# Optimization experiments

Measured on AMD Instinct MI355X. Metric: run time of the kernel, lower is better.

Reference implementation:

```python
import jax, jax.numpy as jnp
import numpy as np

N, M, K, C, FF, H, OUT = 20000, 80000, 48, 64, 256, 4, 64


def _lin(x, w, b):
    return x @ w.T + b


def _bn(x, g, b, eps=1e-5):
    mu = x.mean(0)
    var = x.var(0)
    return (x - mu) * jax.lax.rsqrt(var + eps) * g + b


def setup_inputs() -> dict:
    key = jax.random.key(0)
    ks = jax.random.split(key, 24)
    voxel_features = jax.random.normal(ks[0], (M, C), jnp.float32)
    voxel_coords = jax.random.normal(ks[1], (M, 3), jnp.float32)
    query_coords = jax.random.normal(ks[2], (N, 3), jnp.float32)
    idx = jax.random.randint(ks[3], (N, K), 0, M)
    drop = jax.random.uniform(ks[4], (N, K)) < 0.1
    drop = drop.at[:, 0].set(False)  # keep >=1 valid key per query
    key_indices = jnp.where(drop, -1, idx)
    s = 0.05
    p = lambda i, shp: jax.random.normal(ks[i], shp, jnp.float32) * s
    return {
        "voxel_features": voxel_features,
        "voxel_coords": voxel_coords,
        "query_coords": query_coords,
        "key_indices": key_indices,
        "q_w": p(5, (C, 3)), "q_b": p(6, (C,)),
        "kpos_w": p(7, (C, 3)), "kpos_b": p(8, (C,)),
        "in_w": p(9, (3 * C, C)), "in_b": p(10, (3 * C,)),
        "out_w": p(11, (C, C)), "out_b": p(12, (C,)),
        "lin1_w": p(13, (FF, C)), "lin1_b": p(14, (FF,)),
        "lin2_w": p(15, (C, FF)), "lin2_b": p(16, (C,)),
        "norm_g": jnp.ones((C,), jnp.float32), "norm_b": jnp.zeros((C,), jnp.float32),
        "outl_w": p(17, (OUT, C)), "outl_b": p(18, (OUT,)),
        "obn_g": jnp.ones((OUT,), jnp.float32), "obn_b": jnp.zeros((OUT,), jnp.float32),
    }


def reference(voxel_features, voxel_coords, query_coords, key_indices,
              q_w, q_b, kpos_w, kpos_b, in_w, in_b, out_w, out_b,
              lin1_w, lin1_b, lin2_w, lin2_b, norm_g, norm_b,
              outl_w, outl_b, obn_g, obn_b):
    hd = C // H
    mask = key_indices < 0                      # (N,K) padded keys
    safe = jnp.where(mask, 0, key_indices)
    key_feats = voxel_features[safe]            # (N,K,C) hash-gather
    key_coords = voxel_coords[safe]             # (N,K,3)
    # query positional projection
    q_feat = jax.nn.relu(_lin(query_coords, q_w, q_b))          # (N,C)
    # relative coords + key positional conv1d(kernel=1) == linear on coord dim
    rel = key_coords - query_coords[:, None, :]                  # (N,K,3)
    key_feats = key_feats + jax.nn.relu(_lin(rel, kpos_w, kpos_b))
    # multihead attention, query length 1 per voxel
    Wq, Wk, Wv = jnp.split(in_w, 3, axis=0)
    bq, bk, bv = jnp.split(in_b, 3)
    q = (_lin(q_feat, Wq, bq) / jnp.sqrt(jnp.float32(hd))).reshape(N, H, hd)
    k = _lin(key_feats, Wk, bk).reshape(N, K, H, hd)
    v = _lin(key_feats, Wv, bv).reshape(N, K, H, hd)
    scores = jnp.einsum('nhd,nkhd->nhk', q, k)
    scores = jnp.where(mask[:, None, :], -jnp.inf, scores)
    attn = jax.nn.softmax(scores, axis=-1)
    ctx = jnp.einsum('nhk,nkhd->nhd', attn, v).reshape(N, C)
    att = _lin(ctx, out_w, out_b)                                # (N,C)
    # FFN + residual
    x = att + _lin(jax.nn.relu(_lin(att, lin1_w, lin1_b)), lin2_w, lin2_b)
    x = _bn(x, norm_g, norm_b)
    # output layer: Linear -> BN -> ReLU
    x = jax.nn.relu(_bn(_lin(x, outl_w, outl_b), obn_g, obn_b))
    return x
```

## Files before the change

kernel.cpp:

```cpp
#include <hip/hip_runtime.h>
#include <math.h>

#define N_Q 20000
#define KK 48
#define CC 64
#define FFD 256

#define TW_WOT   0
#define TW_WVT   4096
#define U_L1     16384
#define U_L2     32768
#define U_OL     49152
#define U_WQ     53248
#define U_WK     57344
#define ST_OFF   32768
#define M_OFF    33024
#define VF_OFF   2593024

typedef short bf16x8 __attribute__((ext_vector_type(8)));
typedef float f32x4  __attribute__((ext_vector_type(4)));

__device__ __forceinline__ unsigned f2bf(float f) {
    unsigned u = __float_as_uint(f);
    return (u + 0x7fffu + ((u >> 16) & 1u)) >> 16;
}
__device__ __forceinline__ unsigned pk2(float a, float b) {
    return f2bf(a) | (f2bf(b) << 16);
}
__device__ __forceinline__ float bflo(unsigned u) { return __uint_as_float(u << 16); }
__device__ __forceinline__ float bfhi(unsigned u) { return __uint_as_float(u & 0xffff0000u); }
__device__ __forceinline__ bf16x8 ldfrag(const unsigned short* p) {
    return *(const bf16x8*)p;
}

__global__ void prep_all(const float* __restrict__ in_w,
                         const float* __restrict__ out_w,
                         const float* __restrict__ lin1_w,
                         const float* __restrict__ lin2_w,
                         const float* __restrict__ outl_w,
                         const float* __restrict__ vfeat,
                         float* __restrict__ tw,
                         unsigned short* __restrict__ wsu,
                         unsigned short* __restrict__ vfeat_bf,
                         float* __restrict__ stats)
{
    int t = blockIdx.x * 256 + threadIdx.x;
    if (t < 1280000) {
        float4 v = ((const float4*)vfeat)[t];
        uint2 p; p.x = pk2(v.x, v.y); p.y = pk2(v.z, v.w);
        ((uint2*)vfeat_bf)[t] = p;
        return;
    }
    int u = t - 1280000;
    if (u < 4096) {
        int c = u >> 6, j = u & 63;
        tw[TW_WOT + j*64 + c] = out_w[c*64 + j];
    } else if (u < 8192) {
        int i = u - 4096, cp = i >> 6, c = i & 63;
        tw[TW_WVT + cp*64 + c] = in_w[(128 + c)*64 + cp];
    } else if (u < 24576) {
        int i = u - 8192;
        wsu[U_L1 + i] = (unsigned short)f2bf(lin1_w[i]);
    } else if (u < 40960) {
        int i = u - 24576;
        wsu[U_L2 + i] = (unsigned short)f2bf(lin2_w[i]);
    } else if (u < 45056) {
        int i = u - 40960;
        wsu[U_OL + i] = (unsigned short)f2bf(outl_w[i]);
    } else if (u < 49152) {
        int i = u - 45056;
        wsu[U_WQ + i] = (unsigned short)f2bf(in_w[i]);
    } else if (u < 57344) {
        int v = u - 49152;
        int h = v >> 11, rem = v & 2047, j = rem >> 5, k = rem & 31;
        unsigned short val = 0;
        if (k < 16) val = (unsigned short)f2bf(in_w[(64 + h*16 + k)*64 + j]);
        wsu[U_WK + v] = val;
    } else if (u < 57600) {
        stats[u - 57344] = 0.0f;
    }
}

__global__ __launch_bounds__(256) void m_kernel(
    const float* __restrict__ qcoord, const float* __restrict__ q_w,
    const float* __restrict__ q_b, const float* __restrict__ in_b,
    const unsigned short* __restrict__ wsu, unsigned short* __restrict__ M_all)
{
    __shared__ __align__(16) unsigned short sQF[80*72];
    __shared__ __align__(16) unsigned short sQ[80*72];
    int t = threadIdx.x, base = blockIdx.x * 80;
    int colq = (t*4) & 63;
    float qwv[12];
    #pragma unroll
    for (int j = 0; j < 12; ++j) qwv[j] = q_w[colq*3 + j];
    float4 qb4 = *(const float4*)&q_b[colq];
    #pragma unroll
    for (int i = 0; i < 5; ++i) {
        int e = i*1024 + t*4, r = e >> 6, n = base + r;
        float c0 = qcoord[n*3], c1 = qcoord[n*3+1], c2 = qcoord[n*3+2];
        float f0 = fmaxf(fmaf(qwv[2],  c2, fmaf(qwv[1],  c1, fmaf(qwv[0], c0, qb4.x))), 0.f);
        float f1 = fmaxf(fmaf(qwv[5],  c2, fmaf(qwv[4],  c1, fmaf(qwv[3], c0, qb4.y))), 0.f);
        float f2 = fmaxf(fmaf(qwv[8],  c2, fmaf(qwv[7],  c1, fmaf(qwv[6], c0, qb4.z))), 0.f);
        float f3 = fmaxf(fmaf(qwv[11], c2, fmaf(qwv[10], c1, fmaf(qwv[9], c0, qb4.w))), 0.f);
        uint2 p; p.x = pk2(f0, f1); p.y = pk2(f2, f3);
        *(uint2*)&sQF[r*72 + colq] = p;
    }
    int w = t >> 6, lane = t & 63, l16 = lane & 15, quad = lane >> 4;
    bf16x8 qbf[2], kbf[4];
    #pragma unroll
    for (int ks = 0; ks < 2; ++ks)
        qbf[ks] = ldfrag(&wsu[U_WQ + (w*16 + l16)*64 + ks*32 + quad*8]);
    #pragma unroll
    for (int nb = 0; nb < 4; ++nb)
        kbf[nb] = ldfrag(&wsu[U_WK + w*2048 + (nb*16 + l16)*32 + quad*8]);
    __syncthreads();

    int cq = w*16 + l16;
    float bq = in_b[cq];
    #pragma unroll
    for (int mb = 0; mb < 5; ++mb) {
        bf16x8 a0 = ldfrag(&sQF[(mb*16 + l16)*72 + quad*8]);
        bf16x8 a1 = ldfrag(&sQF[(mb*16 + l16)*72 + 32 + quad*8]);
        f32x4 acc = {0.f, 0.f, 0.f, 0.f};
        acc = __builtin_amdgcn_mfma_f32_16x16x32_bf16(a0, qbf[0], acc, 0, 0, 0);
        acc = __builtin_amdgcn_mfma_f32_16x16x32_bf16(a1, qbf[1], acc, 0, 0, 0);
        #pragma unroll
        for (int reg = 0; reg < 4; ++reg) {
            int row = mb*16 + quad*4 + reg;
            sQ[row*72 + cq] = (unsigned short)f2bf((acc[reg] + bq) * 0.25f);
        }
    }
    #pragma unroll
    for (int mb = 0; mb < 5; ++mb) {
        bf16x8 a = {0,0,0,0,0,0,0,0};
        if (quad < 2) a = ldfrag(&sQ[(mb*16 + l16)*72 + w*16 + quad*8]);
        f32x4 acc[4];
        #pragma unroll
        for (int nb = 0; nb < 4; ++nb) {
            f32x4 z = {0.f, 0.f, 0.f, 0.f};
            acc[nb] = __builtin_amdgcn_mfma_f32_16x16x32_bf16(a, kbf[nb], z, 0, 0, 0);
        }
        #pragma unroll
        for (int nb = 0; nb < 4; ++nb)
            #pragma unroll
            for (int reg = 0; reg < 4; ++reg) {
                int r = base + mb*16 + quad*4 + reg, j = nb*16 + l16;
                M_all[(size_t)r*256 + w*64 + j] = (unsigned short)f2bf(acc[nb][reg]);
            }
    }
}

__global__ __launch_bounds__(64, 4) void attn_kernel(
    const unsigned short* __restrict__ vfeat_bf, const float* __restrict__ vcoord,
    const float* __restrict__ qcoord, const int* __restrict__ kidx,
    const float* __restrict__ kpos_w, const float* __restrict__ kpos_b,
    const float* __restrict__ in_b, const float* __restrict__ out_b,
    const float* __restrict__ tw, const unsigned short* __restrict__ M_all,
    float* __restrict__ att_out)
{
    __shared__ __align__(16) unsigned short skf[KK*72];
    __shared__ __align__(16) float reg1[256];
    int n = blockIdx.x, c = threadIdx.x;
    int l16 = c & 15, h = c >> 4;
    float* sM   = reg1;
    float* sP   = reg1;
    float* sctx = reg1 + 192;
    float* sT   = (float*)skf;

    {
        uint2 mu = ((const uint2*)(M_all + (size_t)n*256))[c];
        float4 mf;
        mf.x = bflo(mu.x); mf.y = bfhi(mu.x);
        mf.z = bflo(mu.y); mf.w = bfhi(mu.y);
        *(float4*)&sM[h*64 + 4*l16] = mf;
    }

    float qc0 = qcoord[n*3+0], qc1 = qcoord[n*3+1], qc2 = qcoord[n*3+2];

    int kread = c < 48 ? c : 47;
    int idxv = kidx[(size_t)n*KK + kread];
    int sfe = idxv < 0 ? 0 : idxv;
    float rl0 = vcoord[sfe*3+0] - qc0;
    float rl1 = vcoord[sfe*3+1] - qc1;
    float rl2 = vcoord[sfe*3+2] - qc2;

    float4 wA  = *(const float4*)(kpos_w + 12*l16 + 0);
    float4 wB  = *(const float4*)(kpos_w + 12*l16 + 4);
    float4 wC  = *(const float4*)(kpos_w + 12*l16 + 8);
    float4 kb4 = *(const float4*)(kpos_b + 4*l16);

    uint2 fv[12];
    #pragma unroll
    for (int i = 0; i < 12; ++i) {
        int row = 4*i + h;
        int si = __shfl(idxv, row);
        si = si < 0 ? 0 : si;
        fv[i] = *(const uint2*)(vfeat_bf + (size_t)si*64 + 4*l16);
    }
    #pragma unroll
    for (int i = 0; i < 12; ++i) {
        int row = 4*i + h;
        float rr0 = __shfl(rl0, row), rr1 = __shfl(rl1, row), rr2 = __shfl(rl2, row);
        float g0 = bflo(fv[i].x), g1 = bfhi(fv[i].x);
        float g2 = bflo(fv[i].y), g3 = bfhi(fv[i].y);
        g0 += fmaxf(fmaf(wA.x, rr0, fmaf(wA.y, rr1, fmaf(wA.z, rr2, kb4.x))), 0.0f);
        g1 += fmaxf(fmaf(wA.w, rr0, fmaf(wB.x, rr1, fmaf(wB.y, rr2, kb4.y))), 0.0f);
        g2 += fmaxf(fmaf(wB.z, rr0, fmaf(wB.w, rr1, fmaf(wC.x, rr2, kb4.z))), 0.0f);
        g3 += fmaxf(fmaf(wC.y, rr0, fmaf(wC.z, rr1, fmaf(wC.w, rr2, kb4.w))), 0.0f);
        uint2 p; p.x = pk2(g0, g1); p.y = pk2(g2, g3);
        *(uint2*)&skf[row*72 + 4*l16] = p;
    }

    int i0 = __shfl(idxv, l16), i1 = __shfl(idxv, l16 + 16), i2 = __shfl(idxv, l16 + 32);
    float S0 = 0, S1 = 0, S2 = 0;
    #pragma unroll
    for (int j8 = 0; j8 < 8; ++j8) {
        uint2 A = *(const uint2*)&skf[ l16       *72 + 8*j8];
        uint2 A2= *(const uint2*)&skf[ l16       *72 + 8*j8 + 4];
        uint2 B = *(const uint2*)&skf[(l16 + 16) *72 + 8*j8];
        uint2 B2= *(const uint2*)&skf[(l16 + 16) *72 + 8*j8 + 4];
        uint2 D = *(const uint2*)&skf[(l16 + 32) *72 + 8*j8];
        uint2 D2= *(const uint2*)&skf[(l16 + 32) *72 + 8*j8 + 4];
        float4 mA = *(const float4*)&sM[h*64 + 8*j8];
        float4 mB = *(const float4*)&sM[h*64 + 8*j8 + 4];
        #pragma unroll
        for (int jj = 0; jj < 8; ++jj) {
            unsigned ua = (jj < 4) ? ((jj < 2) ? A.x : A.y) : ((jj < 6) ? A2.x : A2.y);
            unsigned ub = (jj < 4) ? ((jj < 2) ? B.x : B.y) : ((jj < 6) ? B2.x : B2.y);
            unsigned ud = (jj < 4) ? ((jj < 2) ? D.x : D.y) : ((jj < 6) ? D2.x : D2.y);
            float av = (jj & 1) ? bfhi(ua) : bflo(ua);
            float bv = (jj & 1) ? bfhi(ub) : bflo(ub);
            float dv = (jj & 1) ? bfhi(ud) : bflo(ud);
            float m  = (jj < 4) ? ((jj < 2) ? ((jj & 1) ? mA.y : mA.x) : ((jj & 1) ? mA.w : mA.z))
                                : ((jj < 6) ? ((jj & 1) ? mB.y : mB.x) : ((jj & 1) ? mB.w : mB.z));
            S0 = fmaf(av, m, S0);
            S1 = fmaf(bv, m, S1);
            S2 = fmaf(dv, m, S2);
        }
    }
    if (i0 < 0) S0 = -INFINITY;
    if (i1 < 0) S1 = -INFINITY;
    if (i2 < 0) S2 = -INFINITY;

    float mx = fmaxf(S0, fmaxf(S1, S2));
    #pragma unroll
    for (int off = 8; off >= 1; off >>= 1) mx = fmaxf(mx, __shfl_xor(mx, off, 16));
    float e0 = __expf(S0 - mx), e1 = __expf(S1 - mx), e2 = __expf(S2 - mx);
    float es = e0 + e1 + e2;
    #pragma unroll
    for (int off = 8; off >= 1; off >>= 1) es += __shfl_xor(es, off, 16);
    float rinv = 1.0f / es;
    sP[ l16       *4 + h] = e0 * rinv;
    sP[(l16 + 16) *4 + h] = e1 * rinv;
    sP[(l16 + 32) *4 + h] = e2 * rinv;

    float T0 = 0, T1 = 0, T2 = 0, T3 = 0;
    #pragma unroll 8
    for (int k = 0; k < KK; ++k) {
        float kf = __uint_as_float(((unsigned)skf[k*72 + c]) << 16);
        float4 p = *(const float4*)&sP[k*4];
        T0 = fmaf(p.x, kf, T0); T1 = fmaf(p.y, kf, T1);
        T2 = fmaf(p.z, kf, T2); T3 = fmaf(p.w, kf, T3);
    }
    sT[0*65 + c] = T0; sT[1*65 + c] = T1; sT[2*65 + c] = T2; sT[3*65 + c] = T3;

    const float* WvT = tw + TW_WVT;
    float ctx = in_b[128 + c];
    #pragma unroll 8
    for (int cp = 0; cp < 64; ++cp)
        ctx = fmaf(sT[h*65 + cp], WvT[cp*64 + c], ctx);
    sctx[c] = ctx;

    const float* WoT = tw + TW_WOT;
    float att = out_b[c];
    #pragma unroll 8
    for (int j = 0; j < 64; ++j)
        att = fmaf(sctx[j], WoT[j*64 + c], att);
    att_out[(size_t)n*64 + c] = att;
}

__global__ __launch_bounds__(256) void ffn_kernel(
    const unsigned short* __restrict__ wsu, const float* __restrict__ lin1_b,
    const float* __restrict__ lin2_b, float* __restrict__ att_y,
    float* __restrict__ sum1, float* __restrict__ sumsq1)
{
    __shared__ __align__(16) unsigned short sA[48*72];
    __shared__ __align__(16) unsigned short sH[48*264];
    int t = threadIdx.x, base = blockIdx.x * 48;
    #pragma unroll
    for (int i = 0; i < 3; ++i) {
        int e = i*1024 + t*4, r = e >> 6, col = e & 63;
        int n = base + r;
        uint2 p = {0u, 0u};
        if (n < N_Q) {
            float4 v = *(const float4*)&att_y[(size_t)n*64 + col];
            p.x = pk2(v.x, v.y); p.y = pk2(v.z, v.w);
        }
        *(uint2*)&sA[r*72 + col] = p;
    }
    int w = t >> 6, lane = t & 63, l16 = lane & 15, quad = lane >> 4;
    bf16x8 b1f[2][4], b2f[8];
    #pragma unroll
    for (int ks = 0; ks < 2; ++ks)
        #pragma unroll
        for (int nb = 0; nb < 4; ++nb)
            b1f[ks][nb] = ldfrag(&wsu[U_L1 + (w*64 + nb*16 + l16)*64 + ks*32 + quad*8]);
    #pragma unroll
    for (int ks = 0; ks < 8; ++ks)
        b2f[ks] = ldfrag(&wsu[U_L2 + (w*16 + l16)*256 + ks*32 + quad*8]);
    __syncthreads();

    #pragma unroll
    for (int mb = 0; mb < 3; ++mb) {
        bf16x8 a0 = ldfrag(&sA[(mb*16 + l16)*72 + quad*8]);
        bf16x8 a1 = ldfrag(&sA[(mb*16 + l16)*72 + 32 + quad*8]);
        #pragma unroll
        for (int nb = 0; nb < 4; ++nb) {
            f32x4 acc = {0.f, 0.f, 0.f, 0.f};
            acc = __builtin_amdgcn_mfma_f32_16x16x32_bf16(a0, b1f[0][nb], acc, 0, 0, 0);
            acc = __builtin_amdgcn_mfma_f32_16x16x32_bf16(a1, b1f[1][nb], acc, 0, 0, 0);
            int f = w*64 + nb*16 + l16;
            float bias = lin1_b[f];
            #pragma unroll
            for (int reg = 0; reg < 4; ++reg) {
                int row = mb*16 + quad*4 + reg;
                sH[row*264 + f] = (unsigned short)f2bf(fmaxf(acc[reg] + bias, 0.0f));
            }
        }
    }
    __syncthreads();

    int c = w*16 + l16;
    float lb2 = lin2_b[c];
    float s = 0.f, ss = 0.f;
    #pragma unroll
    for (int mb = 0; mb < 3; ++mb) {
        f32x4 acc = {0.f, 0.f, 0.f, 0.f};
        #pragma unroll
        for (int ks = 0; ks < 8; ++ks) {
            bf16x8 a = ldfrag(&sH[(mb*16 + l16)*264 + ks*32 + quad*8]);
            acc = __builtin_amdgcn_mfma_f32_16x16x32_bf16(a, b2f[ks], acc, 0, 0, 0);
        }
        #pragma unroll
        for (int reg = 0; reg < 4; ++reg) {
            int r = base + mb*16 + quad*4 + reg;
            if (r < N_Q) {
                float y = att_y[(size_t)r*64 + c] + lb2 + acc[reg];
                att_y[(size_t)r*64 + c] = y;
                s += y; ss = fmaf(y, y, ss);
            }
        }
    }
    s  += __shfl_xor(s, 16);  s  += __shfl_xor(s, 32);
    ss += __shfl_xor(ss, 16); ss += __shfl_xor(ss, 32);
    if (lane < 16) {
        atomicAdd(&sum1[c], s);
        atomicAdd(&sumsq1[c], ss);
    }
}

__global__ __launch_bounds__(256) void linout_kernel(
    const unsigned short* __restrict__ wsu, const float* __restrict__ outl_b,
    const float* __restrict__ norm_g, const float* __restrict__ norm_b,
    const float* __restrict__ sum1, const float* __restrict__ sumsq1,
    const float* __restrict__ y, float* __restrict__ z_out,
    float* __restrict__ sum2, float* __restrict__ sumsq2)
{
    __shared__ __align__(16) unsigned short sX[48*72];
    int t = threadIdx.x, base = blockIdx.x * 48;
    int colq = (t*4) & 63;
    const float invN = 1.0f / 20000.0f;
    float4 sm = *(const float4*)&sum1[colq];
    float4 sq = *(const float4*)&sumsq1[colq];
    float4 g  = *(const float4*)&norm_g[colq];
    float4 bb = *(const float4*)&norm_b[colq];
    float mu0 = sm.x*invN, mu1 = sm.y*invN, mu2 = sm.z*invN, mu3 = sm.w*invN;
    float a0 = g.x / sqrtf(fmaf(-mu0, mu0, sq.x*invN) + 1e-5f);
    float a1 = g.y / sqrtf(fmaf(-mu1, mu1, sq.y*invN) + 1e-5f);
    float a2 = g.z / sqrtf(fmaf(-mu2, mu2, sq.z*invN) + 1e-5f);
    float a3 = g.w / sqrtf(fmaf(-mu3, mu3, sq.w*invN) + 1e-5f);
    float b0 = fmaf(-mu0, a0, bb.x), b1 = fmaf(-mu1, a1, bb.y);
    float b2 = fmaf(-mu2, a2, bb.z), b3 = fmaf(-mu3, a3, bb.w);
    #pragma unroll
    for (int i = 0; i < 3; ++i) {
        int e = i*1024 + t*4, r = e >> 6;
        int n = base + r;
        uint2 p = {0u, 0u};
        if (n < N_Q) {
            float4 v = *(const float4*)&y[(size_t)n*64 + colq];
            p.x = pk2(fmaf(v.x, a0, b0), fmaf(v.y, a1, b1));
            p.y = pk2(fmaf(v.z, a2, b2), fmaf(v.w, a3, b3));
        }
        *(uint2*)&sX[r*72 + colq] = p;
    }
    int w = t >> 6, lane = t & 63, l16 = lane & 15, quad = lane >> 4;
    bf16x8 obf[2];
    #pragma unroll
    for (int ks = 0; ks < 2; ++ks)
        obf[ks] = ldfrag(&wsu[U_OL + (w*16 + l16)*64 + ks*32 + quad*8]);
    __syncthreads();

    int co = w*16 + l16;
    float ob = outl_b[co];
    float s = 0.f, ss = 0.f;
    #pragma unroll
    for (int mb = 0; mb < 3; ++mb) {
        bf16x8 x0 = ldfrag(&sX[(mb*16 + l16)*72 + quad*8]);
        bf16x8 x1 = ldfrag(&sX[(mb*16 + l16)*72 + 32 + quad*8]);
        f32x4 acc = {0.f, 0.f, 0.f, 0.f};
        acc = __builtin_amdgcn_mfma_f32_16x16x32_bf16(x0, obf[0], acc, 0, 0, 0);
        acc = __builtin_amdgcn_mfma_f32_16x16x32_bf16(x1, obf[1], acc, 0, 0, 0);
        #pragma unroll
        for (int reg = 0; reg < 4; ++reg) {
            int r = base + mb*16 + quad*4 + reg;
            if (r < N_Q) {
                float zv = acc[reg] + ob;
                z_out[(size_t)r*64 + co] = zv;
                s += zv; ss = fmaf(zv, zv, ss);
            }
        }
    }
    s  += __shfl_xor(s, 16);  s  += __shfl_xor(s, 32);
    ss += __shfl_xor(ss, 16); ss += __shfl_xor(ss, 32);
    if (lane < 16) {
        atomicAdd(&sum2[co], s);
        atomicAdd(&sumsq2[co], ss);
    }
}

__global__ void final_kernel(float* __restrict__ z,
    const float* __restrict__ sum2, const float* __restrict__ sumsq2,
    const float* __restrict__ obn_g, const float* __restrict__ obn_b)
{
    int i = blockIdx.x*blockDim.x + threadIdx.x;
    if (i >= N_Q*64/4) return;
    int o4 = (i*4) & 63;
    float4 sm = *(const float4*)&sum2[o4];
    float4 sq = *(const float4*)&sumsq2[o4];
    float4 g  = *(const float4*)&obn_g[o4];
    float4 b  = *(const float4*)&obn_b[o4];
    const float invN = 1.0f / 20000.0f;
    float mux = sm.x*invN, muy = sm.y*invN, muz = sm.z*invN, muw = sm.w*invN;
    float ax = g.x / sqrtf(fmaf(-mux, mux, sq.x*invN) + 1e-5f);
    float ay = g.y / sqrtf(fmaf(-muy, muy, sq.y*invN) + 1e-5f);
    float az = g.z / sqrtf(fmaf(-muz, muz, sq.z*invN) + 1e-5f);
    float aw = g.w / sqrtf(fmaf(-muw, muw, sq.w*invN) + 1e-5f);
    float4 v = ((float4*)z)[i];
    v.x = fmaxf(fmaf(v.x - mux, ax, b.x), 0.0f);
    v.y = fmaxf(fmaf(v.y - muy, ay, b.y), 0.0f);
    v.z = fmaxf(fmaf(v.z - muz, az, b.z), 0.0f);
    v.w = fmaxf(fmaf(v.w - muw, aw, b.w), 0.0f);
    ((float4*)z)[i] = v;
}

extern "C" void kernel_launch(void* const* d_in, const int* in_sizes, int n_in,
                              void* d_out, int out_size, void* d_ws, size_t ws_size,
                              hipStream_t stream)
{
    const float* vfeat  = (const float*)d_in[0];
    const float* vcoord = (const float*)d_in[1];
    const float* qcoord = (const float*)d_in[2];
    const int*   kidx   = (const int*)d_in[3];
    const float* q_w    = (const float*)d_in[4];
    const float* q_b    = (const float*)d_in[5];
    const float* kpos_w = (const float*)d_in[6];
    const float* kpos_b = (const float*)d_in[7];
    const float* in_w   = (const float*)d_in[8];
    const float* in_b   = (const float*)d_in[9];
    const float* out_w  = (const float*)d_in[10];
    const float* out_b  = (const float*)d_in[11];
    const float* lin1_w = (const float*)d_in[12];
    const float* lin1_b = (const float*)d_in[13];
    const float* lin2_w = (const float*)d_in[14];
    const float* lin2_b = (const float*)d_in[15];
    const float* norm_g = (const float*)d_in[16];
    const float* norm_b = (const float*)d_in[17];
    const float* outl_w = (const float*)d_in[18];
    const float* outl_b = (const float*)d_in[19];
    const float* obn_g  = (const float*)d_in[20];
    const float* obn_b  = (const float*)d_in[21];

    float* ws = (float*)d_ws;
    float* tw = ws;
    unsigned short* wsu = (unsigned short*)ws;
    float* stats = ws + ST_OFF;
    float* sum1 = stats, *sumsq1 = stats + 64, *sum2 = stats + 128, *sumsq2 = stats + 192;
    unsigned short* M_all = (unsigned short*)(ws + M_OFF);
    unsigned short* vfeat_bf = (unsigned short*)(ws + VF_OFF);
    float* xd = (float*)d_out;

    prep_all<<<5225, 256, 0, stream>>>(in_w, out_w, lin1_w, lin2_w, outl_w,
                                       vfeat, tw, wsu, vfeat_bf, stats);
    m_kernel<<<250, 256, 0, stream>>>(qcoord, q_w, q_b, in_b, wsu, M_all);
    attn_kernel<<<N_Q, 64, 0, stream>>>(vfeat_bf, vcoord, qcoord, kidx, kpos_w, kpos_b,
                                        in_b, out_b, tw, M_all, xd);
    ffn_kernel<<<417, 256, 0, stream>>>(wsu, lin1_b, lin2_b, xd, sum1, sumsq1);
    linout_kernel<<<417, 256, 0, stream>>>(wsu, outl_b, norm_g, norm_b, sum1, sumsq1,
                                           xd, xd, sum2, sumsq2);
    final_kernel<<<1250, 256, 0, stream>>>(xd, sum2, sumsq2, obn_g, obn_b);
}
```

Before: 208.6 us.

## Shrink row tiles to raise block count and interleave M layout by head

The m_kernel, ffn_kernel and linout_kernel now process 32 or 16 rows per block instead of 80 or 48, which launches more blocks so the small kernels cover more compute units; the bounds checks go away because 20000 divides evenly. The M matrix is stored with heads interleaved (j*4+h), so attn_kernel writes it contiguously and reads one scalar per step from shared memory instead of selecting from float4 vectors. Weight fragments are reloaded more often in total, and there are more atomics on the statistics buffers. The scalar shared-memory reads may cost more LDS instructions or bank conflicts.

```diff
diff --git a/kernel.cpp b/kernel.cpp
--- a/kernel.cpp
+++ b/kernel.cpp
@@ -86,16 +86,16 @@
     const float* __restrict__ q_b, const float* __restrict__ in_b,
     const unsigned short* __restrict__ wsu, unsigned short* __restrict__ M_all)
 {
-    __shared__ __align__(16) unsigned short sQF[80*72];
-    __shared__ __align__(16) unsigned short sQ[80*72];
-    int t = threadIdx.x, base = blockIdx.x * 80;
+    __shared__ __align__(16) unsigned short sQF[32*72];
+    __shared__ __align__(16) unsigned short sQ[32*72];
+    int t = threadIdx.x, base = blockIdx.x * 32;
     int colq = (t*4) & 63;
     float qwv[12];
     #pragma unroll
     for (int j = 0; j < 12; ++j) qwv[j] = q_w[colq*3 + j];
     float4 qb4 = *(const float4*)&q_b[colq];
     #pragma unroll
-    for (int i = 0; i < 5; ++i) {
+    for (int i = 0; i < 2; ++i) {
         int e = i*1024 + t*4, r = e >> 6, n = base + r;
         float c0 = qcoord[n*3], c1 = qcoord[n*3+1], c2 = qcoord[n*3+2];
         float f0 = fmaxf(fmaf(qwv[2],  c2, fmaf(qwv[1],  c1, fmaf(qwv[0], c0, qb4.x))), 0.f);
@@ -118,7 +118,7 @@
     int cq = w*16 + l16;
     float bq = in_b[cq];
     #pragma unroll
-    for (int mb = 0; mb < 5; ++mb) {
+    for (int mb = 0; mb < 2; ++mb) {
         bf16x8 a0 = ldfrag(&sQF[(mb*16 + l16)*72 + quad*8]);
         bf16x8 a1 = ldfrag(&sQF[(mb*16 + l16)*72 + 32 + quad*8]);
         f32x4 acc = {0.f, 0.f, 0.f, 0.f};
@@ -131,7 +131,7 @@
         }
     }
     #pragma unroll
-    for (int mb = 0; mb < 5; ++mb) {
+    for (int mb = 0; mb < 2; ++mb) {
         bf16x8 a = {0,0,0,0,0,0,0,0};
         if (quad < 2) a = ldfrag(&sQ[(mb*16 + l16)*72 + w*16 + quad*8]);
         f32x4 acc[4];
@@ -145,7 +145,7 @@
             #pragma unroll
             for (int reg = 0; reg < 4; ++reg) {
                 int r = base + mb*16 + quad*4 + reg, j = nb*16 + l16;
-                M_all[(size_t)r*256 + w*64 + j] = (unsigned short)f2bf(acc[nb][reg]);
+                M_all[(size_t)r*256 + j*4 + w] = (unsigned short)f2bf(acc[nb][reg]);
             }
     }
 }
@@ -172,7 +172,7 @@
         float4 mf;
         mf.x = bflo(mu.x); mf.y = bfhi(mu.x);
         mf.z = bflo(mu.y); mf.w = bfhi(mu.y);
-        *(float4*)&sM[h*64 + 4*l16] = mf;
+        *(float4*)&sM[4*c] = mf;
     }
 
     float qc0 = qcoord[n*3+0], qc1 = qcoord[n*3+1], qc2 = qcoord[n*3+2];
@@ -221,8 +221,6 @@
         uint2 B2= *(const uint2*)&skf[(l16 + 16) *72 + 8*j8 + 4];
         uint2 D = *(const uint2*)&skf[(l16 + 32) *72 + 8*j8];
         uint2 D2= *(const uint2*)&skf[(l16 + 32) *72 + 8*j8 + 4];
-        float4 mA = *(const float4*)&sM[h*64 + 8*j8];
-        float4 mB = *(const float4*)&sM[h*64 + 8*j8 + 4];
         #pragma unroll
         for (int jj = 0; jj < 8; ++jj) {
             unsigned ua = (jj < 4) ? ((jj < 2) ? A.x : A.y) : ((jj < 6) ? A2.x : A2.y);
@@ -231,8 +229,7 @@
             float av = (jj & 1) ? bfhi(ua) : bflo(ua);
             float bv = (jj & 1) ? bfhi(ub) : bflo(ub);
             float dv = (jj & 1) ? bfhi(ud) : bflo(ud);
-            float m  = (jj < 4) ? ((jj < 2) ? ((jj & 1) ? mA.y : mA.x) : ((jj & 1) ? mA.w : mA.z))
-                                : ((jj < 6) ? ((jj & 1) ? mB.y : mB.x) : ((jj & 1) ? mB.w : mB.z));
+            float m  = sM[(8*j8 + jj)*4 + h];
             S0 = fmaf(av, m, S0);
             S1 = fmaf(bv, m, S1);
             S2 = fmaf(dv, m, S2);
@@ -284,18 +281,13 @@
     const float* __restrict__ lin2_b, float* __restrict__ att_y,
     float* __restrict__ sum1, float* __restrict__ sumsq1)
 {
-    __shared__ __align__(16) unsigned short sA[48*72];
-    __shared__ __align__(16) unsigned short sH[48*264];
-    int t = threadIdx.x, base = blockIdx.x * 48;
-    #pragma unroll
-    for (int i = 0; i < 3; ++i) {
-        int e = i*1024 + t*4, r = e >> 6, col = e & 63;
-        int n = base + r;
-        uint2 p = {0u, 0u};
-        if (n < N_Q) {
-            float4 v = *(const float4*)&att_y[(size_t)n*64 + col];
-            p.x = pk2(v.x, v.y); p.y = pk2(v.z, v.w);
-        }
+    __shared__ __align__(16) unsigned short sA[16*72];
+    __shared__ __align__(16) unsigned short sH[16*264];
+    int t = threadIdx.x, base = blockIdx.x * 16;
+    {
+        int e = t*4, r = e >> 6, col = e & 63;
+        float4 v = *(const float4*)&att_y[(size_t)(base + r)*64 + col];
+        uint2 p; p.x = pk2(v.x, v.y); p.y = pk2(v.z, v.w);
         *(uint2*)&sA[r*72 + col] = p;
     }
     int w = t >> 6, lane = t & 63, l16 = lane & 15, quad = lane >> 4;
@@ -310,10 +302,9 @@
         b2f[ks] = ldfrag(&wsu[U_L2 + (w*16 + l16)*256 + ks*32 + quad*8]);
     __syncthreads();
 
-    #pragma unroll
-    for (int mb = 0; mb < 3; ++mb) {
-        bf16x8 a0 = ldfrag(&sA[(mb*16 + l16)*72 + quad*8]);
-        bf16x8 a1 = ldfrag(&sA[(mb*16 + l16)*72 + 32 + quad*8]);
+    {
+        bf16x8 a0 = ldfrag(&sA[l16*72 + quad*8]);
+        bf16x8 a1 = ldfrag(&sA[l16*72 + 32 + quad*8]);
         #pragma unroll
         for (int nb = 0; nb < 4; ++nb) {
             f32x4 acc = {0.f, 0.f, 0.f, 0.f};
@@ -322,10 +313,8 @@
             int f = w*64 + nb*16 + l16;
             float bias = lin1_b[f];
             #pragma unroll
-            for (int reg = 0; reg < 4; ++reg) {
-                int row = mb*16 + quad*4 + reg;
-                sH[row*264 + f] = (unsigned short)f2bf(fmaxf(acc[reg] + bias, 0.0f));
-            }
+            for (int reg = 0; reg < 4; ++reg)
+                sH[(quad*4 + reg)*264 + f] = (unsigned short)f2bf(fmaxf(acc[reg] + bias, 0.0f));
         }
     }
     __syncthreads();
@@ -333,22 +322,19 @@
     int c = w*16 + l16;
     float lb2 = lin2_b[c];
     float s = 0.f, ss = 0.f;
-    #pragma unroll
-    for (int mb = 0; mb < 3; ++mb) {
+    {
         f32x4 acc = {0.f, 0.f, 0.f, 0.f};
         #pragma unroll
         for (int ks = 0; ks < 8; ++ks) {
-            bf16x8 a = ldfrag(&sH[(mb*16 + l16)*264 + ks*32 + quad*8]);
+            bf16x8 a = ldfrag(&sH[l16*264 + ks*32 + quad*8]);
             acc = __builtin_amdgcn_mfma_f32_16x16x32_bf16(a, b2f[ks], acc, 0, 0, 0);
         }
         #pragma unroll
         for (int reg = 0; reg < 4; ++reg) {
-            int r = base + mb*16 + quad*4 + reg;
-            if (r < N_Q) {
-                float y = att_y[(size_t)r*64 + c] + lb2 + acc[reg];
-                att_y[(size_t)r*64 + c] = y;
-                s += y; ss = fmaf(y, y, ss);
-            }
+            int r = base + quad*4 + reg;
+            float y = att_y[(size_t)r*64 + c] + lb2 + acc[reg];
+            att_y[(size_t)r*64 + c] = y;
+            s += y; ss = fmaf(y, y, ss);
         }
     }
     s  += __shfl_xor(s, 16);  s  += __shfl_xor(s, 32);
@@ -366,8 +352,8 @@
     const float* __restrict__ y, float* __restrict__ z_out,
     float* __restrict__ sum2, float* __restrict__ sumsq2)
 {
-    __shared__ __align__(16) unsigned short sX[48*72];
-    int t = threadIdx.x, base = blockIdx.x * 48;
+    __shared__ __align__(16) unsigned short sX[16*72];
+    int t = threadIdx.x, base = blockIdx.x * 16;
     int colq = (t*4) & 63;
     const float invN = 1.0f / 20000.0f;
     float4 sm = *(const float4*)&sum1[colq];
@@ -381,16 +367,12 @@
     float a3 = g.w / sqrtf(fmaf(-mu3, mu3, sq.w*invN) + 1e-5f);
     float b0 = fmaf(-mu0, a0, bb.x), b1 = fmaf(-mu1, a1, bb.y);
     float b2 = fmaf(-mu2, a2, bb.z), b3 = fmaf(-mu3, a3, bb.w);
-    #pragma unroll
-    for (int i = 0; i < 3; ++i) {
-        int e = i*1024 + t*4, r = e >> 6;
-        int n = base + r;
-        uint2 p = {0u, 0u};
-        if (n < N_Q) {
-            float4 v = *(const float4*)&y[(size_t)n*64 + colq];
-            p.x = pk2(fmaf(v.x, a0, b0), fmaf(v.y, a1, b1));
-            p.y = pk2(fmaf(v.z, a2, b2), fmaf(v.w, a3, b3));
-        }
+    {
+        int e = t*4, r = e >> 6;
+        float4 v = *(const float4*)&y[(size_t)(base + r)*64 + colq];
+        uint2 p;
+        p.x = pk2(fmaf(v.x, a0, b0), fmaf(v.y, a1, b1));
+        p.y = pk2(fmaf(v.z, a2, b2), fmaf(v.w, a3, b3));
         *(uint2*)&sX[r*72 + colq] = p;
     }
     int w = t >> 6, lane = t & 63, l16 = lane & 15, quad = lane >> 4;
@@ -403,21 +385,18 @@
     int co = w*16 + l16;
     float ob = outl_b[co];
     float s = 0.f, ss = 0.f;
-    #pragma unroll
-    for (int mb = 0; mb < 3; ++mb) {
-        bf16x8 x0 = ldfrag(&sX[(mb*16 + l16)*72 + quad*8]);
-        bf16x8 x1 = ldfrag(&sX[(mb*16 + l16)*72 + 32 + quad*8]);
+    {
+        bf16x8 x0 = ldfrag(&sX[l16*72 + quad*8]);
+        bf16x8 x1 = ldfrag(&sX[l16*72 + 32 + quad*8]);
         f32x4 acc = {0.f, 0.f, 0.f, 0.f};
         acc = __builtin_amdgcn_mfma_f32_16x16x32_bf16(x0, obf[0], acc, 0, 0, 0);
         acc = __builtin_amdgcn_mfma_f32_16x16x32_bf16(x1, obf[1], acc, 0, 0, 0);
         #pragma unroll
         for (int reg = 0; reg < 4; ++reg) {
-            int r = base + mb*16 + quad*4 + reg;
-            if (r < N_Q) {
-                float zv = acc[reg] + ob;
-                z_out[(size_t)r*64 + co] = zv;
-                s += zv; ss = fmaf(zv, zv, ss);
-            }
+            int r = base + quad*4 + reg;
+            float zv = acc[reg] + ob;
+            z_out[(size_t)r*64 + co] = zv;
+            s += zv; ss = fmaf(zv, zv, ss);
         }
     }
     s  += __shfl_xor(s, 16);  s  += __shfl_xor(s, 32);
@@ -491,11 +470,11 @@
 
     prep_all<<<5225, 256, 0, stream>>>(in_w, out_w, lin1_w, lin2_w, outl_w,
                                        vfeat, tw, wsu, vfeat_bf, stats);
-    m_kernel<<<250, 256, 0, stream>>>(qcoord, q_w, q_b, in_b, wsu, M_all);
+    m_kernel<<<625, 256, 0, stream>>>(qcoord, q_w, q_b, in_b, wsu, M_all);
     attn_kernel<<<N_Q, 64, 0, stream>>>(vfeat_bf, vcoord, qcoord, kidx, kpos_w, kpos_b,
                                         in_b, out_b, tw, M_all, xd);
-    ffn_kernel<<<417, 256, 0, stream>>>(wsu, lin1_b, lin2_b, xd, sum1, sumsq1);
-    linout_kernel<<<417, 256, 0, stream>>>(wsu, outl_b, norm_g, norm_b, sum1, sumsq1,
-                                           xd, xd, sum2, sumsq2);
+    ffn_kernel<<<1250, 256, 0, stream>>>(wsu, lin1_b, lin2_b, xd, sum1, sumsq1);
+    linout_kernel<<<1250, 256, 0, stream>>>(wsu, outl_b, norm_g, norm_b, sum1, sumsq1,
+                                            xd, xd, sum2, sumsq2);
     final_kernel<<<1250, 256, 0, stream>>>(xd, sum2, sumsq2, obn_g, obn_b);
 }
```

Result: slower. 249.3 us (+19.5%).

## Fold both batchnorms into output linear via covariance statistics, merge prep kernels

Applied to the files above, without the earlier changes.

Merges the weight-prep and M kernels into one launch, and builds the Wq/Wk bf16 fragments directly from in_w. The FFN kernel now also accumulates the 64x64 second-moment matrix of its output with MFMA. A single-block stats kernel uses it to compute the output-BN mean and variance analytically, then folds both batchnorms and the output bias into one scaled weight matrix and bias. The output linear, BN and ReLU thus become a single pass, removing the separate linout and final kernels and a full read/write of the activations. The output BN variance now comes from a bf16 covariance, which risks reduced accuracy. The M layout is also interleaved by head for attn_kernel's reads.

```diff
diff --git a/kernel.cpp b/kernel.cpp
--- a/kernel.cpp
+++ b/kernel.cpp
@@ -8,14 +8,12 @@
 
 #define TW_WOT   0
 #define TW_WVT   4096
+#define ST_F     24576
 #define U_L1     16384
 #define U_L2     32768
-#define U_OL     49152
-#define U_WQ     53248
-#define U_WK     57344
-#define ST_OFF   32768
-#define M_OFF    33024
-#define VF_OFF   2593024
+#define U_W2     57600
+#define U_M      61696
+#define U_VF     5181696
 
 typedef short bf16x8 __attribute__((ext_vector_type(8)));
 typedef float f32x4  __attribute__((ext_vector_type(4)));
@@ -32,71 +30,63 @@
 __device__ __forceinline__ bf16x8 ldfrag(const unsigned short* p) {
     return *(const bf16x8*)p;
 }
-
-__global__ void prep_all(const float* __restrict__ in_w,
-                         const float* __restrict__ out_w,
-                         const float* __restrict__ lin1_w,
-                         const float* __restrict__ lin2_w,
-                         const float* __restrict__ outl_w,
-                         const float* __restrict__ vfeat,
-                         float* __restrict__ tw,
-                         unsigned short* __restrict__ wsu,
-                         unsigned short* __restrict__ vfeat_bf,
-                         float* __restrict__ stats)
-{
-    int t = blockIdx.x * 256 + threadIdx.x;
-    if (t < 1280000) {
-        float4 v = ((const float4*)vfeat)[t];
-        uint2 p; p.x = pk2(v.x, v.y); p.y = pk2(v.z, v.w);
-        ((uint2*)vfeat_bf)[t] = p;
-        return;
-    }
-    int u = t - 1280000;
-    if (u < 4096) {
-        int c = u >> 6, j = u & 63;
-        tw[TW_WOT + j*64 + c] = out_w[c*64 + j];
-    } else if (u < 8192) {
-        int i = u - 4096, cp = i >> 6, c = i & 63;
-        tw[TW_WVT + cp*64 + c] = in_w[(128 + c)*64 + cp];
-    } else if (u < 24576) {
-        int i = u - 8192;
-        wsu[U_L1 + i] = (unsigned short)f2bf(lin1_w[i]);
-    } else if (u < 40960) {
-        int i = u - 24576;
-        wsu[U_L2 + i] = (unsigned short)f2bf(lin2_w[i]);
-    } else if (u < 45056) {
-        int i = u - 40960;
-        wsu[U_OL + i] = (unsigned short)f2bf(outl_w[i]);
-    } else if (u < 49152) {
-        int i = u - 45056;
-        wsu[U_WQ + i] = (unsigned short)f2bf(in_w[i]);
-    } else if (u < 57344) {
-        int v = u - 49152;
-        int h = v >> 11, rem = v & 2047, j = rem >> 5, k = rem & 31;
-        unsigned short val = 0;
-        if (k < 16) val = (unsigned short)f2bf(in_w[(64 + h*16 + k)*64 + j]);
-        wsu[U_WK + v] = val;
-    } else if (u < 57600) {
-        stats[u - 57344] = 0.0f;
-    }
-}
-
-__global__ __launch_bounds__(256) void m_kernel(
+__device__ __forceinline__ bf16x8 pack8(float4 a, float4 b) {
+    union { unsigned u[4]; bf16x8 v; } r;
+    r.u[0] = pk2(a.x, a.y); r.u[1] = pk2(a.z, a.w);
+    r.u[2] = pk2(b.x, b.y); r.u[3] = pk2(b.z, b.w);
+    return r.v;
+}
+
+__global__ __launch_bounds__(256) void prep_m(
+    const float* __restrict__ in_w,  const float* __restrict__ out_w,
+    const float* __restrict__ lin1_w, const float* __restrict__ lin2_w,
+    const float* __restrict__ vfeat,
     const float* __restrict__ qcoord, const float* __restrict__ q_w,
-    const float* __restrict__ q_b, const float* __restrict__ in_b,
-    const unsigned short* __restrict__ wsu, unsigned short* __restrict__ M_all)
+    const float* __restrict__ q_b,   const float* __restrict__ in_b,
+    float* __restrict__ tw, unsigned short* __restrict__ wsu,
+    unsigned short* __restrict__ vfeat_bf, float* __restrict__ stats,
+    unsigned short* __restrict__ M_all)
 {
     __shared__ __align__(16) unsigned short sQF[80*72];
     __shared__ __align__(16) unsigned short sQ[80*72];
-    int t = threadIdx.x, base = blockIdx.x * 80;
-    int colq = (t*4) & 63;
+    int b = blockIdx.x, tid = threadIdx.x;
+
+    if (b < 5000) {
+        int i = b*256 + tid;
+        float4 v = ((const float4*)vfeat)[i];
+        uint2 p; p.x = pk2(v.x, v.y); p.y = pk2(v.z, v.w);
+        ((uint2*)vfeat_bf)[i] = p;
+        return;
+    }
+    if (b < 5177) {
+        int u = (b - 5000)*256 + tid;
+        if (u < 4096) {
+            int c = u >> 6, j = u & 63;
+            tw[TW_WOT + j*64 + c] = out_w[c*64 + j];
+        } else if (u < 8192) {
+            int i = u - 4096, cp = i >> 6, c = i & 63;
+            tw[TW_WVT + cp*64 + c] = in_w[(128 + c)*64 + cp];
+        } else if (u < 24576) {
+            int i = u - 8192;
+            wsu[U_L1 + i] = (unsigned short)f2bf(lin1_w[i]);
+        } else if (u < 40960) {
+            int i = u - 24576;
+            wsu[U_L2 + i] = (unsigned short)f2bf(lin2_w[i]);
+        } else if (u < 45184) {
+            stats[u - 40960] = 0.0f;
+        }
+        return;
+    }
+
+    int base = (b - 5177) * 80;
+    int colq = (tid*4) & 63;
     float qwv[12];
     #pragma unroll
     for (int j = 0; j < 12; ++j) qwv[j] = q_w[colq*3 + j];
     float4 qb4 = *(const float4*)&q_b[colq];
     #pragma unroll
     for (int i = 0; i < 5; ++i) {
-        int e = i*1024 + t*4, r = e >> 6, n = base + r;
+        int e = i*1024 + tid*4, r = e >> 6, n = base + r;
         float c0 = qcoord[n*3], c1 = qcoord[n*3+1], c2 = qcoord[n*3+2];
         float f0 = fmaxf(fmaf(qwv[2],  c2, fmaf(qwv[1],  c1, fmaf(qwv[0], c0, qb4.x))), 0.f);
         float f1 = fmaxf(fmaf(qwv[5],  c2, fmaf(qwv[4],  c1, fmaf(qwv[3], c0, qb4.y))), 0.f);
@@ -105,14 +95,29 @@
         uint2 p; p.x = pk2(f0, f1); p.y = pk2(f2, f3);
         *(uint2*)&sQF[r*72 + colq] = p;
     }
-    int w = t >> 6, lane = t & 63, l16 = lane & 15, quad = lane >> 4;
+    int w = tid >> 6, lane = tid & 63, l16 = lane & 15, quad = lane >> 4;
+
     bf16x8 qbf[2], kbf[4];
     #pragma unroll
-    for (int ks = 0; ks < 2; ++ks)
-        qbf[ks] = ldfrag(&wsu[U_WQ + (w*16 + l16)*64 + ks*32 + quad*8]);
-    #pragma unroll
-    for (int nb = 0; nb < 4; ++nb)
-        kbf[nb] = ldfrag(&wsu[U_WK + w*2048 + (nb*16 + l16)*32 + quad*8]);
+    for (int ks = 0; ks < 2; ++ks) {
+        const float4* p = (const float4*)(in_w + (w*16 + l16)*64 + ks*32 + quad*8);
+        qbf[ks] = pack8(p[0], p[1]);
+    }
+    #pragma unroll
+    for (int nb = 0; nb < 4; ++nb) {
+        union { unsigned u[4]; bf16x8 v; } r;
+        if (quad < 2) {
+            float f[8];
+            #pragma unroll
+            for (int jj = 0; jj < 8; ++jj)
+                f[jj] = in_w[(64 + w*16 + quad*8 + jj)*64 + nb*16 + l16];
+            r.u[0] = pk2(f[0], f[1]); r.u[1] = pk2(f[2], f[3]);
+            r.u[2] = pk2(f[4], f[5]); r.u[3] = pk2(f[6], f[7]);
+        } else {
+            r.u[0] = r.u[1] = r.u[2] = r.u[3] = 0u;
+        }
+        kbf[nb] = r.v;
+    }
     __syncthreads();
 
     int cq = w*16 + l16;
@@ -145,7 +150,7 @@
             #pragma unroll
             for (int reg = 0; reg < 4; ++reg) {
                 int r = base + mb*16 + quad*4 + reg, j = nb*16 + l16;
-                M_all[(size_t)r*256 + w*64 + j] = (unsigned short)f2bf(acc[nb][reg]);
+                M_all[(size_t)r*256 + j*4 + w] = (unsigned short)f2bf(acc[nb][reg]);
             }
     }
 }
@@ -172,11 +177,10 @@
         float4 mf;
         mf.x = bflo(mu.x); mf.y = bfhi(mu.x);
         mf.z = bflo(mu.y); mf.w = bfhi(mu.y);
-        *(float4*)&sM[h*64 + 4*l16] = mf;
+        *(float4*)&sM[4*c] = mf;
     }
 
     float qc0 = qcoord[n*3+0], qc1 = qcoord[n*3+1], qc2 = qcoord[n*3+2];
-
     int kread = c < 48 ? c : 47;
     int idxv = kidx[(size_t)n*KK + kread];
     int sfe = idxv < 0 ? 0 : idxv;
@@ -221,8 +225,6 @@
         uint2 B2= *(const uint2*)&skf[(l16 + 16) *72 + 8*j8 + 4];
         uint2 D = *(const uint2*)&skf[(l16 + 32) *72 + 8*j8];
         uint2 D2= *(const uint2*)&skf[(l16 + 32) *72 + 8*j8 + 4];
-        float4 mA = *(const float4*)&sM[h*64 + 8*j8];
-        float4 mB = *(const float4*)&sM[h*64 + 8*j8 + 4];
         #pragma unroll
         for (int jj = 0; jj < 8; ++jj) {
             unsigned ua = (jj < 4) ? ((jj < 2) ? A.x : A.y) : ((jj < 6) ? A2.x : A2.y);
@@ -231,8 +233,7 @@
             float av = (jj & 1) ? bfhi(ua) : bflo(ua);
             float bv = (jj & 1) ? bfhi(ub) : bflo(ub);
             float dv = (jj & 1) ? bfhi(ud) : bflo(ud);
-            float m  = (jj < 4) ? ((jj < 2) ? ((jj & 1) ? mA.y : mA.x) : ((jj & 1) ? mA.w : mA.z))
-                                : ((jj < 6) ? ((jj & 1) ? mB.y : mB.x) : ((jj & 1) ? mB.w : mB.z));
+            float m  = sM[(8*j8 + jj)*4 + h];
             S0 = fmaf(av, m, S0);
             S1 = fmaf(bv, m, S1);
             S2 = fmaf(dv, m, S2);
@@ -282,20 +283,18 @@
 __global__ __launch_bounds__(256) void ffn_kernel(
     const unsigned short* __restrict__ wsu, const float* __restrict__ lin1_b,
     const float* __restrict__ lin2_b, float* __restrict__ att_y,
-    float* __restrict__ sum1, float* __restrict__ sumsq1)
+    float* __restrict__ sum1, float* __restrict__ Syy)
 {
-    __shared__ __align__(16) unsigned short sA[48*72];
-    __shared__ __align__(16) unsigned short sH[48*264];
-    int t = threadIdx.x, base = blockIdx.x * 48;
-    #pragma unroll
-    for (int i = 0; i < 3; ++i) {
+    __shared__ __align__(16) unsigned short uni[64*104];
+    __shared__ __align__(16) unsigned short sH[80*264];
+    unsigned short* sA  = uni;
+    unsigned short* sYT = uni;
+    int t = threadIdx.x, base = blockIdx.x * 80;
+    #pragma unroll
+    for (int i = 0; i < 5; ++i) {
         int e = i*1024 + t*4, r = e >> 6, col = e & 63;
-        int n = base + r;
-        uint2 p = {0u, 0u};
-        if (n < N_Q) {
-            float4 v = *(const float4*)&att_y[(size_t)n*64 + col];
-            p.x = pk2(v.x, v.y); p.y = pk2(v.z, v.w);
-        }
+        float4 v = *(const float4*)&att_y[(size_t)(base + r)*64 + col];
+        uint2 p; p.x = pk2(v.x, v.y); p.y = pk2(v.z, v.w);
         *(uint2*)&sA[r*72 + col] = p;
     }
     int w = t >> 6, lane = t & 63, l16 = lane & 15, quad = lane >> 4;
@@ -311,7 +310,7 @@
     __syncthreads();
 
     #pragma unroll
-    for (int mb = 0; mb < 3; ++mb) {
+    for (int mb = 0; mb < 5; ++mb) {
         bf16x8 a0 = ldfrag(&sA[(mb*16 + l16)*72 + quad*8]);
         bf16x8 a1 = ldfrag(&sA[(mb*16 + l16)*72 + 32 + quad*8]);
         #pragma unroll
@@ -332,125 +331,142 @@
 
     int c = w*16 + l16;
     float lb2 = lin2_b[c];
-    float s = 0.f, ss = 0.f;
-    #pragma unroll
-    for (int mb = 0; mb < 3; ++mb) {
+    float s = 0.f;
+    #pragma unroll
+    for (int mb = 0; mb < 5; ++mb) {
         f32x4 acc = {0.f, 0.f, 0.f, 0.f};
         #pragma unroll
         for (int ks = 0; ks < 8; ++ks) {
             bf16x8 a = ldfrag(&sH[(mb*16 + l16)*264 + ks*32 + quad*8]);
             acc = __builtin_amdgcn_mfma_f32_16x16x32_bf16(a, b2f[ks], acc, 0, 0, 0);
         }
+        float y4[4];
         #pragma unroll
         for (int reg = 0; reg < 4; ++reg) {
             int r = base + mb*16 + quad*4 + reg;
-            if (r < N_Q) {
-                float y = att_y[(size_t)r*64 + c] + lb2 + acc[reg];
-                att_y[(size_t)r*64 + c] = y;
-                s += y; ss = fmaf(y, y, ss);
-            }
-        }
-    }
-    s  += __shfl_xor(s, 16);  s  += __shfl_xor(s, 32);
-    ss += __shfl_xor(ss, 16); ss += __shfl_xor(ss, 32);
-    if (lane < 16) {
-        atomicAdd(&sum1[c], s);
-        atomicAdd(&sumsq1[c], ss);
-    }
-}
-
-__global__ __launch_bounds__(256) void linout_kernel(
-    const unsigned short* __restrict__ wsu, const float* __restrict__ outl_b,
-    const float* __restrict__ norm_g, const float* __restrict__ norm_b,
-    const float* __restrict__ sum1, const float* __restrict__ sumsq1,
-    const float* __restrict__ y, float* __restrict__ z_out,
-    float* __restrict__ sum2, float* __restrict__ sumsq2)
+            float y = att_y[(size_t)r*64 + c] + lb2 + acc[reg];
+            att_y[(size_t)r*64 + c] = y;
+            y4[reg] = y;
+            s += y;
+        }
+        uint2 p; p.x = pk2(y4[0], y4[1]); p.y = pk2(y4[2], y4[3]);
+        *(uint2*)&sYT[c*104 + mb*16 + quad*4] = p;
+    }
+    {
+        uint2 z = {0u, 0u};
+        *(uint2*)&sYT[c*104 + 80 + quad*4] = z;
+    }
+    s += __shfl_xor(s, 16); s += __shfl_xor(s, 32);
+    if (lane < 16) atomicAdd(&sum1[c], s);
+    __syncthreads();
+
+    f32x4 accS[4] = {{0,0,0,0},{0,0,0,0},{0,0,0,0},{0,0,0,0}};
+    #pragma unroll
+    for (int ks = 0; ks < 3; ++ks) {
+        bf16x8 af = ldfrag(&sYT[(w*16 + l16)*104 + ks*32 + quad*8]);
+        #pragma unroll
+        for (int nb = 0; nb < 4; ++nb) {
+            bf16x8 bfr = ldfrag(&sYT[(nb*16 + l16)*104 + ks*32 + quad*8]);
+            accS[nb] = __builtin_amdgcn_mfma_f32_16x16x32_bf16(af, bfr, accS[nb], 0, 0, 0);
+        }
+    }
+    #pragma unroll
+    for (int nb = 0; nb < 4; ++nb)
+        #pragma unroll
+        for (int reg = 0; reg < 4; ++reg)
+            atomicAdd(&Syy[(w*16 + quad*4 + reg)*64 + nb*16 + l16], accS[nb][reg]);
+}
+
+__global__ __launch_bounds__(256) void stats_kernel(
+    const float* __restrict__ sum1, const float* __restrict__ SyyG,
+    const float* __restrict__ outl_w, const float* __restrict__ norm_g,
+    const float* __restrict__ obn_g, const float* __restrict__ obn_b,
+    unsigned short* __restrict__ W2, float* __restrict__ Cb)
 {
-    __shared__ __align__(16) unsigned short sX[48*72];
-    int t = threadIdx.x, base = blockIdx.x * 48;
-    int colq = (t*4) & 63;
+    __shared__ float sSyy[64*64];
+    __shared__ float sOlf[64*65];
+    __shared__ float sMu[64], sSc[64], sM1[64];
+    int t = threadIdx.x;
     const float invN = 1.0f / 20000.0f;
-    float4 sm = *(const float4*)&sum1[colq];
-    float4 sq = *(const float4*)&sumsq1[colq];
-    float4 g  = *(const float4*)&norm_g[colq];
-    float4 bb = *(const float4*)&norm_b[colq];
-    float mu0 = sm.x*invN, mu1 = sm.y*invN, mu2 = sm.z*invN, mu3 = sm.w*invN;
-    float a0 = g.x / sqrtf(fmaf(-mu0, mu0, sq.x*invN) + 1e-5f);
-    float a1 = g.y / sqrtf(fmaf(-mu1, mu1, sq.y*invN) + 1e-5f);
-    float a2 = g.z / sqrtf(fmaf(-mu2, mu2, sq.z*invN) + 1e-5f);
-    float a3 = g.w / sqrtf(fmaf(-mu3, mu3, sq.w*invN) + 1e-5f);
-    float b0 = fmaf(-mu0, a0, bb.x), b1 = fmaf(-mu1, a1, bb.y);
-    float b2 = fmaf(-mu2, a2, bb.z), b3 = fmaf(-mu3, a3, bb.w);
-    #pragma unroll
-    for (int i = 0; i < 3; ++i) {
-        int e = i*1024 + t*4, r = e >> 6;
-        int n = base + r;
-        uint2 p = {0u, 0u};
-        if (n < N_Q) {
-            float4 v = *(const float4*)&y[(size_t)n*64 + colq];
-            p.x = pk2(fmaf(v.x, a0, b0), fmaf(v.y, a1, b1));
-            p.y = pk2(fmaf(v.z, a2, b2), fmaf(v.w, a3, b3));
-        }
-        *(uint2*)&sX[r*72 + colq] = p;
+    for (int i = t; i < 4096; i += 256) sSyy[i] = SyyG[i];
+    __syncthreads();
+    if (t < 64) {
+        float mu = sum1[t] * invN;
+        float var = sSyy[t*64 + t]*invN - mu*mu;
+        sMu[t] = mu;
+        sSc[t] = norm_g[t] / sqrtf(var + 1e-5f);
+    }
+    __syncthreads();
+    for (int i = t; i < 4096; i += 256) {
+        int o = i >> 6, c = i & 63;
+        sOlf[o*65 + c] = outl_w[i] * sSc[c];
+    }
+    __syncthreads();
+    if (t < 64) {
+        float m1 = 0;
+        for (int c = 0; c < 64; ++c) m1 += sOlf[t*65 + c] * sMu[c];
+        sM1[t] = m1;
+    }
+    __syncthreads();
+    int o = t >> 2, cp0 = (t & 3) * 16;
+    float qp = 0;
+    for (int cp = cp0; cp < cp0 + 16; ++cp) {
+        float t2 = 0;
+        for (int c = 0; c < 64; ++c) t2 += sOlf[o*65 + c] * sSyy[c*64 + cp];
+        qp += t2 * sOlf[o*65 + cp];
+    }
+    qp += __shfl_xor(qp, 1);
+    qp += __shfl_xor(qp, 2);
+    __syncthreads();
+    if ((t & 3) == 0) {
+        float m1 = sM1[o];
+        float varz = qp*invN - m1*m1;
+        float a2 = obn_g[o] / sqrtf(varz + 1e-5f);
+        sSc[o] = a2;
+        Cb[o] = obn_b[o] - m1*a2;
+    }
+    __syncthreads();
+    for (int i = t; i < 4096; i += 256) {
+        int oo = i >> 6, c = i & 63;
+        W2[i] = (unsigned short)f2bf(sOlf[oo*65 + c] * sSc[oo]);
+    }
+}
+
+__global__ __launch_bounds__(256) void out_kernel(
+    const unsigned short* __restrict__ W2, const float* __restrict__ Cb,
+    float* __restrict__ yz)
+{
+    __shared__ __align__(16) unsigned short sX[80*72];
+    int t = threadIdx.x, base = blockIdx.x * 80;
+    #pragma unroll
+    for (int i = 0; i < 5; ++i) {
+        int e = i*1024 + t*4, r = e >> 6, col = e & 63;
+        float4 v = *(const float4*)&yz[(size_t)(base + r)*64 + col];
+        uint2 p; p.x = pk2(v.x, v.y); p.y = pk2(v.z, v.w);
+        *(uint2*)&sX[r*72 + col] = p;
     }
     int w = t >> 6, lane = t & 63, l16 = lane & 15, quad = lane >> 4;
-    bf16x8 obf[2];
+    bf16x8 bf[2];
     #pragma unroll
     for (int ks = 0; ks < 2; ++ks)
-        obf[ks] = ldfrag(&wsu[U_OL + (w*16 + l16)*64 + ks*32 + quad*8]);
-    __syncthreads();
-
-    int co = w*16 + l16;
-    float ob = outl_b[co];
-    float s = 0.f, ss = 0.f;
-    #pragma unroll
-    for (int mb = 0; mb < 3; ++mb) {
+        bf[ks] = ldfrag(&W2[(w*16 + l16)*64 + ks*32 + quad*8]);
+    int o = w*16 + l16;
+    float Co = Cb[o];
+    __syncthreads();
+
+    #pragma unroll
+    for (int mb = 0; mb < 5; ++mb) {
         bf16x8 x0 = ldfrag(&sX[(mb*16 + l16)*72 + quad*8]);
         bf16x8 x1 = ldfrag(&sX[(mb*16 + l16)*72 + 32 + quad*8]);
         f32x4 acc = {0.f, 0.f, 0.f, 0.f};
-        acc = __builtin_amdgcn_mfma_f32_16x16x32_bf16(x0, obf[0], acc, 0, 0, 0);
-        acc = __builtin_amdgcn_mfma_f32_16x16x32_bf16(x1, obf[1], acc, 0, 0, 0);
+        acc = __builtin_amdgcn_mfma_f32_16x16x32_bf16(x0, bf[0], acc, 0, 0, 0);
+        acc = __builtin_amdgcn_mfma_f32_16x16x32_bf16(x1, bf[1], acc, 0, 0, 0);
         #pragma unroll
         for (int reg = 0; reg < 4; ++reg) {
             int r = base + mb*16 + quad*4 + reg;
-            if (r < N_Q) {
-                float zv = acc[reg] + ob;
-                z_out[(size_t)r*64 + co] = zv;
-                s += zv; ss = fmaf(zv, zv, ss);
-            }
-        }
-    }
-    s  += __shfl_xor(s, 16);  s  += __shfl_xor(s, 32);
-    ss += __shfl_xor(ss, 16); ss += __shfl_xor(ss, 32);
-    if (lane < 16) {
-        atomicAdd(&sum2[co], s);
-        atomicAdd(&sumsq2[co], ss);
-    }
-}
-
-__global__ void final_kernel(float* __restrict__ z,
-    const float* __restrict__ sum2, const float* __restrict__ sumsq2,
-    const float* __restrict__ obn_g, const float* __restrict__ obn_b)
-{
-    int i = blockIdx.x*blockDim.x + threadIdx.x;
-    if (i >= N_Q*64/4) return;
-    int o4 = (i*4) & 63;
-    float4 sm = *(const float4*)&sum2[o4];
-    float4 sq = *(const float4*)&sumsq2[o4];
-    float4 g  = *(const float4*)&obn_g[o4];
-    float4 b  = *(const float4*)&obn_b[o4];
-    const float invN = 1.0f / 20000.0f;
-    float mux = sm.x*invN, muy = sm.y*invN, muz = sm.z*invN, muw = sm.w*invN;
-    float ax = g.x / sqrtf(fmaf(-mux, mux, sq.x*invN) + 1e-5f);
-    float ay = g.y / sqrtf(fmaf(-muy, muy, sq.y*invN) + 1e-5f);
-    float az = g.z / sqrtf(fmaf(-muz, muz, sq.z*invN) + 1e-5f);
-    float aw = g.w / sqrtf(fmaf(-muw, muw, sq.w*invN) + 1e-5f);
-    float4 v = ((float4*)z)[i];
-    v.x = fmaxf(fmaf(v.x - mux, ax, b.x), 0.0f);
-    v.y = fmaxf(fmaf(v.y - muy, ay, b.y), 0.0f);
-    v.z = fmaxf(fmaf(v.z - muz, az, b.z), 0.0f);
-    v.w = fmaxf(fmaf(v.w - muw, aw, b.w), 0.0f);
-    ((float4*)z)[i] = v;
+            yz[(size_t)r*64 + o] = fmaxf(acc[reg] + Co, 0.0f);
+        }
+    }
 }
 
 extern "C" void kernel_launch(void* const* d_in, const int* in_sizes, int n_in,
@@ -474,28 +490,28 @@
     const float* lin2_w = (const float*)d_in[14];
     const float* lin2_b = (const float*)d_in[15];
     const float* norm_g = (const float*)d_in[16];
-    const float* norm_b = (const float*)d_in[17];
     const float* outl_w = (const float*)d_in[18];
-    const float* outl_b = (const float*)d_in[19];
     const float* obn_g  = (const float*)d_in[20];
     const float* obn_b  = (const float*)d_in[21];
 
     float* ws = (float*)d_ws;
     float* tw = ws;
     unsigned short* wsu = (unsigned short*)ws;
-    float* stats = ws + ST_OFF;
-    float* sum1 = stats, *sumsq1 = stats + 64, *sum2 = stats + 128, *sumsq2 = stats + 192;
-    unsigned short* M_all = (unsigned short*)(ws + M_OFF);
-    unsigned short* vfeat_bf = (unsigned short*)(ws + VF_OFF);
+    float* stats = ws + ST_F;
+    float* sum1 = stats;
+    float* Syy  = stats + 64;
+    float* Cb   = stats + 4160;
+    unsigned short* W2 = wsu + U_W2;
+    unsigned short* M_all = wsu + U_M;
+    unsigned short* vfeat_bf = wsu + U_VF;
     float* xd = (float*)d_out;
 
-    prep_all<<<5225, 256, 0, stream>>>(in_w, out_w, lin1_w, lin2_w, outl_w,
-                                       vfeat, tw, wsu, vfeat_bf, stats);
-    m_kernel<<<250, 256, 0, stream>>>(qcoord, q_w, q_b, in_b, wsu, M_all);
+    prep_m<<<5427, 256, 0, stream>>>(in_w, out_w, lin1_w, lin2_w, vfeat,
+                                     qcoord, q_w, q_b, in_b,
+                                     tw, wsu, vfeat_bf, stats, M_all);
     attn_kernel<<<N_Q, 64, 0, stream>>>(vfeat_bf, vcoord, qcoord, kidx, kpos_w, kpos_b,
                                         in_b, out_b, tw, M_all, xd);
-    ffn_kernel<<<417, 256, 0, stream>>>(wsu, lin1_b, lin2_b, xd, sum1, sumsq1);
-    linout_kernel<<<417, 256, 0, stream>>>(wsu, outl_b, norm_g, norm_b, sum1, sumsq1,
-                                           xd, xd, sum2, sumsq2);
-    final_kernel<<<1250, 256, 0, stream>>>(xd, sum2, sumsq2, obn_g, obn_b);
-}
+    ffn_kernel<<<250, 256, 0, stream>>>(wsu, lin1_b, lin2_b, xd, sum1, Syy);
+    stats_kernel<<<1, 256, 0, stream>>>(sum1, Syy, outl_w, norm_g, obn_g, obn_b, W2, Cb);
+    out_kernel<<<250, 256, 0, stream>>>(W2, Cb, xd);
+}
```

After: 230.3 us. 10.4% more time.
